# Kernel optimization log

Hardware: AMD Instinct MI355X
Metric: run time of the kernel (lower is better)

Reference implementation:

```python
import jax, jax.numpy as jnp
import numpy as np

DIM, H, KVH = 1024, 16, 4
HD = DIM // H            # head_dim = 64
KV_DIM = KVH * HD        # 256
ROPE_BASE = 10000.0
EPS = 1e-6


def setup_inputs() -> dict:
    key = jax.random.key(0)
    ks = jax.random.split(key, 6)
    B, S = 4, 2048
    x = jax.random.normal(ks[0], (B, S, DIM), dtype=jnp.float32)
    sc = 0.02
    Wq = jax.random.normal(ks[1], (DIM, DIM), dtype=jnp.float32) * sc
    Wk = jax.random.normal(ks[2], (KV_DIM, DIM), dtype=jnp.float32) * sc
    Wv = jax.random.normal(ks[3], (KV_DIM, DIM), dtype=jnp.float32) * sc
    Wo = jax.random.normal(ks[4], (DIM, DIM), dtype=jnp.float32) * sc
    q_gain = jnp.full((H,), 1.5, dtype=jnp.float32)
    return {"x": x, "Wq": Wq, "Wk": Wk, "Wv": Wv, "Wo": Wo, "q_gain": q_gain}


def _rms_norm(t):
    return t * jax.lax.rsqrt(jnp.mean(t * t, axis=-1, keepdims=True) + EPS)


def _rotary(seqlen, dtype):
    inv_freq = 1.0 / (ROPE_BASE ** (jnp.arange(0, HD, 2, dtype=jnp.float32) / HD))
    t = jnp.arange(seqlen, dtype=jnp.float32)
    freqs = jnp.outer(t, inv_freq)                      # [S, HD/2]
    return jnp.cos(freqs).astype(dtype)[None, None], jnp.sin(freqs).astype(dtype)[None, None]


def _apply_rot(t, cos, sin):
    half = t.shape[-1] // 2
    t1, t2 = t[..., :half], t[..., half:]
    return jnp.concatenate((t1 * cos + t2 * sin, -t1 * sin + t2 * cos), axis=-1)


def reference(x, Wq, Wk, Wv, Wo, q_gain):
    B, S, D = x.shape
    q = (x @ Wq.T).reshape(B, S, H, HD).transpose(0, 2, 1, 3)      # [B,H,S,HD]
    k = (x @ Wk.T).reshape(B, S, KVH, HD).transpose(0, 2, 1, 3)    # [B,KVH,S,HD]
    v = (x @ Wv.T).reshape(B, S, KVH, HD).transpose(0, 2, 1, 3)
    q, k = _rms_norm(q), _rms_norm(k)
    cos, sin = _rotary(S, q.dtype)
    q, k = _apply_rot(q, cos, sin), _apply_rot(k, cos, sin)
    q = q * q_gain.astype(q.dtype)[None, :, None, None]
    rep = H // KVH
    k_exp = jnp.repeat(k, rep, axis=1)                              # GQA expand
    v_exp = jnp.repeat(v, rep, axis=1)
    scores = jnp.einsum('bhqd,bhkd->bhqk', q, k_exp) / np.sqrt(HD)
    causal = jnp.tril(jnp.ones((S, S), dtype=bool))
    scores = jnp.where(causal[None, None], scores, jnp.finfo(scores.dtype).min)
    attn = jax.nn.softmax(scores, axis=-1)
    y = jnp.einsum('bhqk,bhkd->bhqd', attn, v_exp)
    y = y.transpose(0, 2, 1, 3).reshape(B, S, D)
    return y @ Wo.T
```

## Files before the change

### kernel.cpp

```cpp
#include <hip/hip_runtime.h>

typedef float f32x4 __attribute__((ext_vector_type(4)));
typedef float f32x16 __attribute__((ext_vector_type(16)));
typedef __bf16 bf16x8 __attribute__((ext_vector_type(8)));
typedef unsigned short u16x8 __attribute__((ext_vector_type(8)));
typedef int i32x2 __attribute__((ext_vector_type(2)));
typedef int i32x4 __attribute__((ext_vector_type(4)));

#define DEV static __device__ __forceinline__

DEV float bf2f(unsigned short h) {
  unsigned int u = ((unsigned int)h) << 16;
  return __builtin_bit_cast(float, u);
}
DEV unsigned short f2bf(float f) {
  unsigned int u = __builtin_bit_cast(unsigned int, f);
  u += 0x7fff + ((u >> 16) & 1);
  return (unsigned short)(u >> 16);
}

DEV void g2l16(const void* g, void* l) {
  __builtin_amdgcn_global_load_lds(
      (const __attribute__((address_space(1))) void*)g,
      (__attribute__((address_space(3))) void*)l, 16, 0, 0);
}

DEV unsigned int cvtpk(float lo, float hi) {
  unsigned int r;
  asm("v_cvt_pk_bf16_f32 %0, %1, %2" : "=v"(r) : "v"(lo), "v"(hi));
  return r;
}

DEV float fexp2(float x) {
  float r;
  asm("v_exp_f32 %0, %1" : "=v"(r) : "v"(x));
  return r;
}

DEV void cvt8(const float* __restrict__ in, unsigned short* __restrict__ out, int idx) {
  int i = idx * 8;
  float4 a = *(const float4*)(in + i);
  float4 b = *(const float4*)(in + i + 4);
  u16x8 r;
  r[0] = f2bf(a.x); r[1] = f2bf(a.y); r[2] = f2bf(a.z); r[3] = f2bf(a.w);
  r[4] = f2bf(b.x); r[5] = f2bf(b.y); r[6] = f2bf(b.z); r[7] = f2bf(b.w);
  *(u16x8*)(out + i) = r;
}

__global__ __launch_bounds__(256) void k_cvt_all(const float* __restrict__ x,
                                                 const float* __restrict__ wq,
                                                 const float* __restrict__ wk,
                                                 const float* __restrict__ wv,
                                                 const float* __restrict__ wo,
                                                 unsigned short* __restrict__ xb,
                                                 unsigned short* __restrict__ wcat,
                                                 unsigned short* __restrict__ wob,
                                                 float2* __restrict__ rope) {
  const int blk = blockIdx.x, tid = threadIdx.x;
  if (blk < 4096) {
    cvt8(x, xb, blk * 256 + tid);
  } else if (blk < 4608) {
    cvt8(wq, wcat, (blk - 4096) * 256 + tid);
  } else if (blk < 4736) {
    cvt8(wk, wcat + 1048576, (blk - 4608) * 256 + tid);
  } else if (blk < 4864) {
    cvt8(wv, wcat + 1310720, (blk - 4736) * 256 + tid);
  } else if (blk < 5376) {
    cvt8(wo, wob, (blk - 4864) * 256 + tid);
  } else {
    int idx = (blk - 5376) * 256 + tid;
    int s = idx >> 5, dmod = idx & 31;
    float inv_freq = powf(10000.0f, -(float)dmod * (1.0f / 32.0f));
    float sn, cs;
    sincosf((float)s * inv_freq, &sn, &cs);
    rope[idx] = make_float2(cs, sn);
  }
}

__global__ __launch_bounds__(256) void k_qkv(const unsigned short* __restrict__ A,
                                             const unsigned short* __restrict__ B,
                                             const float* __restrict__ qg,
                                             const float2* __restrict__ rope,
                                             unsigned short* __restrict__ qn,
                                             unsigned short* __restrict__ kn2,
                                             unsigned short* __restrict__ vt2) {
  __shared__ unsigned short LDS[16384];
  unsigned short* As = LDS;
  unsigned short* Bs = LDS + 8192;
  const int K = 1024;
  const int tid = threadIdx.x;
  const int wid = tid >> 6, lane = tid & 63;
  const int g = lane >> 4, r16 = lane & 15;
  const int m0 = blockIdx.x * 128;
  const int y = blockIdx.y;
  const int n0 = y * 128;
  const int wr = wid >> 1, wc = wid & 1;

  f32x4 acc[4][4];
#pragma unroll
  for (int i = 0; i < 4; ++i)
#pragma unroll
    for (int j = 0; j < 4; ++j) acc[i][j] = f32x4{0.f, 0.f, 0.f, 0.f};

  const int cb = (lane & 7) * 16;

  for (int k0 = 0; k0 < K; k0 += 64) {
#pragma unroll
    for (int c = 0; c < 4; ++c) {
      int i = wid * 4 + c;
      int row = i * 8 + (lane >> 3);
      int sc = cb ^ ((row & 7) << 4);
      g2l16((const char*)A + ((size_t)(m0 + row) * K + k0) * 2 + sc, (char*)As + i * 1024);
      g2l16((const char*)B + ((size_t)(n0 + row) * K + k0) * 2 + sc, (char*)Bs + i * 1024);
    }
    __syncthreads();
#pragma unroll
    for (int kh = 0; kh < 2; ++kh) {
      bf16x8 af[4], bfr[4];
#pragma unroll
      for (int m = 0; m < 4; ++m) {
        int row = wr * 64 + m * 16 + r16;
        int byte = row * 128 + ((g * 16 + kh * 64) ^ ((row & 7) << 4));
        af[m] = *(const bf16x8*)((const char*)As + byte);
      }
#pragma unroll
      for (int n = 0; n < 4; ++n) {
        int row = wc * 64 + n * 16 + r16;
        int byte = row * 128 + ((g * 16 + kh * 64) ^ ((row & 7) << 4));
        bfr[n] = *(const bf16x8*)((const char*)Bs + byte);
      }
#pragma unroll
      for (int m = 0; m < 4; ++m)
#pragma unroll
        for (int n = 0; n < 4; ++n)
          acc[m][n] = __builtin_amdgcn_mfma_f32_16x16x32_bf16(af[m], bfr[n], acc[m][n], 0, 0, 0);
    }
    __syncthreads();
  }

  if (y < 10) {
    const bool isq = (y < 8);
    const int head = isq ? (2 * y + wc) : (2 * (y - 8) + wc);
    const float gain = isq ? qg[head] * 0.18033688011112042f : 1.0f;
    unsigned short* T = LDS;
#pragma unroll
    for (int m = 0; m < 4; ++m)
#pragma unroll
      for (int j = 0; j < 4; ++j) {
        int tokl = wr * 64 + m * 16 + g * 4 + j;
        int tok = m0 + tokl;
        int s = tok & 2047;
        float v0 = acc[m][0][j], v1 = acc[m][1][j], v2 = acc[m][2][j], v3 = acc[m][3][j];
        float ss = v0 * v0 + v1 * v1 + v2 * v2 + v3 * v3;
        ss += __shfl_xor(ss, 1); ss += __shfl_xor(ss, 2);
        ss += __shfl_xor(ss, 4); ss += __shfl_xor(ss, 8);
        float rs = rsqrtf(ss * (1.0f / 64.0f) + 1e-6f) * gain;
        float2 cs0 = rope[s * 32 + r16];
        float2 cs1 = rope[s * 32 + 16 + r16];
        float o0 = (v0 * cs0.x + v2 * cs0.y) * rs;
        float o2 = (v2 * cs0.x - v0 * cs0.y) * rs;
        float o1 = (v1 * cs1.x + v3 * cs1.y) * rs;
        float o3 = (v3 * cs1.x - v1 * cs1.y) * rs;
        char* rowb = (char*)T + tokl * 256;
        const int sw = (tokl & 15) << 4;
        const int dbase = wc * 128 + r16 * 2;
        *(unsigned short*)(rowb + ((dbase) ^ sw)) = f2bf(o0);
        *(unsigned short*)(rowb + ((dbase + 32) ^ sw)) = f2bf(o1);
        *(unsigned short*)(rowb + ((dbase + 64) ^ sw)) = f2bf(o2);
        *(unsigned short*)(rowb + ((dbase + 96) ^ sw)) = f2bf(o3);
      }
    __syncthreads();
    if (isq) {
      const int row0 = tid >> 4, cl = tid & 15;
      unsigned short* dstb = qn + 2 * y * 64;
#pragma unroll
      for (int it = 0; it < 8; ++it) {
        int row = it * 16 + row0;
        i32x4 w = *(const i32x4*)((const char*)T + row * 256 + ((cl * 16) ^ ((row & 15) << 4)));
        *(i32x4*)(dstb + (size_t)(m0 + row) * 1024 + cl * 8) = w;
      }
    } else {
      const int b_ = m0 >> 11;
      const int kb0 = (m0 & 2047) >> 5;
      const int fu = tid >> 3, sub = tid & 7;
      const int hsel = fu >> 4, kb = (fu >> 2) & 3, m = fu & 3;
      const int headk = 2 * (y - 8) + hsel;
      unsigned short* dst =
          kn2 + ((size_t)((b_ * 4 + headk) * 64 + kb0 + kb) * 4 + m) * 512;
#pragma unroll
      for (int k = 0; k < 8; ++k) {
        int slot = k * 8 + sub;
        int kw = slot & 31, hi8 = slot >> 5;
        int tokl = kb * 32 + kw;
        int d0 = hsel * 64 + m * 16 + hi8 * 8;
        i32x4 w = *(const i32x4*)((const char*)T + tokl * 256 + ((d0 * 2) ^ ((tokl & 15) << 4)));
        *(i32x4*)(dst + slot * 8) = w;
      }
    }
  } else {
    unsigned short* T = LDS;
#pragma unroll
    for (int m = 0; m < 4; ++m)
#pragma unroll
      for (int n = 0; n < 4; ++n)
#pragma unroll
        for (int j = 0; j < 4; ++j) {
          int tokl = wr * 64 + m * 16 + g * 4 + j;
          int dl = wc * 64 + n * 16 + r16;
          int byte = (dl * 256 + tokl * 2) ^ ((dl & 15) << 4);
          *(unsigned short*)((char*)T + byte) = f2bf(acc[m][n][j]);
        }
    __syncthreads();
    const int d = tid >> 1, th = tid & 1;
    const int hv = 2 * (y - 10) + (d >> 6), dh = d & 63;
    const int bb = m0 >> 11;
    const int s0 = (m0 & 2047) + th * 64;
    const int kb64 = s0 >> 6;
    const int db = dh >> 5, d31 = dh & 31;
    const size_t vb0 = ((size_t)(bb * 4 + hv) * 32 + kb64) * 8 + db * 4;
    const int swz = (d & 15) << 4;
#pragma unroll
    for (int c = 0; c < 8; ++c) {
      i32x4 w = *(const i32x4*)((const char*)T + ((d * 256 + th * 128 + c * 16) ^ swz));
      *(i32x4*)(vt2 + (vb0 + (c >> 1)) * 512 + ((c & 1) * 32 + d31) * 8) = w;
    }
  }
}

__global__ __launch_bounds__(256) void k_gemm_bt(const unsigned short* __restrict__ A,
                                                 const unsigned short* __restrict__ B,
                                                 float* __restrict__ C, int M, int N, int K) {
  __shared__ unsigned short As[128 * 64];
  __shared__ unsigned short Bs[128 * 64];
  const int tid = threadIdx.x;
  const int wid = tid >> 6, lane = tid & 63;
  const int g = lane >> 4, r16 = lane & 15;
  const int m0 = blockIdx.x * 128, n0 = blockIdx.y * 128;
  const int wr = wid >> 1, wc = wid & 1;

  f32x4 acc[4][4];
#pragma unroll
  for (int i = 0; i < 4; ++i)
#pragma unroll
    for (int j = 0; j < 4; ++j) acc[i][j] = f32x4{0.f, 0.f, 0.f, 0.f};

  const int cb = (lane & 7) * 16;

  for (int k0 = 0; k0 < K; k0 += 64) {
#pragma unroll
    for (int c = 0; c < 4; ++c) {
      int i = wid * 4 + c;
      int row = i * 8 + (lane >> 3);
      int sc = cb ^ ((row & 7) << 4);
      g2l16((const char*)A + ((size_t)(m0 + row) * K + k0) * 2 + sc, (char*)As + i * 1024);
      g2l16((const char*)B + ((size_t)(n0 + row) * K + k0) * 2 + sc, (char*)Bs + i * 1024);
    }
    __syncthreads();
#pragma unroll
    for (int kh = 0; kh < 2; ++kh) {
      bf16x8 af[4], bfr[4];
#pragma unroll
      for (int m = 0; m < 4; ++m) {
        int row = wr * 64 + m * 16 + r16;
        int byte = row * 128 + ((g * 16 + kh * 64) ^ ((row & 7) << 4));
        af[m] = *(const bf16x8*)((const char*)As + byte);
      }
#pragma unroll
      for (int n = 0; n < 4; ++n) {
        int row = wc * 64 + n * 16 + r16;
        int byte = row * 128 + ((g * 16 + kh * 64) ^ ((row & 7) << 4));
        bfr[n] = *(const bf16x8*)((const char*)Bs + byte);
      }
#pragma unroll
      for (int m = 0; m < 4; ++m)
#pragma unroll
        for (int n = 0; n < 4; ++n)
          acc[m][n] = __builtin_amdgcn_mfma_f32_16x16x32_bf16(af[m], bfr[n], acc[m][n], 0, 0, 0);
    }
    __syncthreads();
  }
#pragma unroll
  for (int m = 0; m < 4; ++m)
#pragma unroll
    for (int n = 0; n < 4; ++n)
#pragma unroll
      for (int j = 0; j < 4; ++j) {
        int row = m0 + wr * 64 + m * 16 + g * 4 + j;
        int col = n0 + wc * 64 + n * 16 + r16;
        C[(size_t)row * N + col] = acc[m][n][j];
      }
}

__global__ __launch_bounds__(512) void k_attn2(const unsigned short* __restrict__ qn,
                                               const unsigned short* __restrict__ kn2,
                                               const unsigned short* __restrict__ vt2,
                                               unsigned short* __restrict__ yb) {
  __shared__ unsigned short SMEM[4 * 8192];
  const int tid = threadIdx.x;
  const int wid = tid >> 6, lane = tid & 63;
  const int hi = lane >> 5, l31 = lane & 31;
  const int flat = blockIdx.x;
  const int qcx = 7 - (flat >> 6);
  const int bh = flat & 63;
  const int b = bh >> 4, h = bh & 15, hv = h >> 2;
  const int q0w = qcx * 256 + wid * 32;
  const int qglob = q0w + l31;
  const int tdiag = (q0w + 31) >> 6;
  const size_t tok0 = (size_t)b * 2048;

  const u16x8 onesu = {0x3F80, 0x3F80, 0x3F80, 0x3F80, 0x3F80, 0x3F80, 0x3F80, 0x3F80};
  const bf16x8 ones = __builtin_bit_cast(bf16x8, onesu);

  bf16x8 qf[4];
#pragma unroll
  for (int m = 0; m < 4; ++m)
    qf[m] = *(const bf16x8*)(qn + (tok0 + qglob) * 1024 + h * 64 + m * 16 + hi * 8);

  f32x16 oacc[2], lacc, zer;
#pragma unroll
  for (int r = 0; r < 16; ++r) { oacc[0][r] = 0.f; oacc[1][r] = 0.f; lacc[r] = 0.f; zer[r] = 0.f; }

  const int c0 = wid * 2;
  const unsigned short* src0;
  if (wid < 4) {
    src0 = kn2 + (size_t)(b * 4 + hv) * 131072 + c0 * 512 + lane * 8;
  } else {
    src0 = vt2 + (size_t)(b * 4 + hv) * 131072 + (c0 - 8) * 512 + lane * 8;
  }
  const unsigned short* src1 = src0 + 512;

  auto stage = [&](int T, int tb) {
    char* dst = (char*)SMEM + tb * 16384 + c0 * 1024;
    g2l16(src0 + (size_t)T * 4096, dst);
    g2l16(src1 + (size_t)T * 4096, dst + 1024);
  };

  const char* lbase = (const char*)SMEM + lane * 16;

  auto qk_tile = [&](int tb, f32x16* s) {
    const char* base = lbase + tb * 16384;
#pragma unroll
    for (int kt = 0; kt < 2; ++kt) {
      __builtin_amdgcn_s_setprio(1);
      bf16x8 kf = *(const bf16x8*)(base + (kt * 4) * 1024);
      f32x16 a = __builtin_amdgcn_mfma_f32_32x32x16_bf16(kf, qf[0], zer, 0, 0, 0);
#pragma unroll
      for (int m = 1; m < 4; ++m) {
        kf = *(const bf16x8*)(base + (kt * 4 + m) * 1024);
        a = __builtin_amdgcn_mfma_f32_32x32x16_bf16(kf, qf[m], a, 0, 0, 0);
      }
      __builtin_amdgcn_s_setprio(0);
      s[kt] = a;
    }
  };

  auto mask_tile = [&](int t, f32x16* s) {
    const int k0 = t * 64;
#pragma unroll
    for (int kt = 0; kt < 2; ++kt)
#pragma unroll
      for (int r = 0; r < 16; ++r) {
        int key = k0 + kt * 32 + (r & 3) + 8 * (r >> 2) + 4 * hi;
        if (key > qglob) s[kt][r] = -INFINITY;
      }
  };

  auto softmax_cvt = [&](f32x16* s, i32x4* paw) {
#pragma unroll
    for (int kt = 0; kt < 2; ++kt)
#pragma unroll
      for (int r = 0; r < 16; ++r) s[kt][r] = fexp2(s[kt][r]);
#pragma unroll
    for (int kt = 0; kt < 2; ++kt)
#pragma unroll
      for (int half = 0; half < 2; ++half) {
        int bs = half * 8;
        unsigned int a0 = cvtpk(s[kt][bs + 0], s[kt][bs + 1]);
        unsigned int a1 = cvtpk(s[kt][bs + 2], s[kt][bs + 3]);
        unsigned int b0 = cvtpk(s[kt][bs + 4], s[kt][bs + 5]);
        unsigned int b1 = cvtpk(s[kt][bs + 6], s[kt][bs + 7]);
        i32x2 r0 = __builtin_amdgcn_permlane32_swap((int)a0, (int)b0, false, false);
        i32x2 r1 = __builtin_amdgcn_permlane32_swap((int)a1, (int)b1, false, false);
        i32x4 w;
        w[0] = r0[0]; w[1] = r1[0]; w[2] = r0[1]; w[3] = r1[1];
        paw[kt * 2 + half] = w;
      }
  };

  auto pv_tile = [&](int tb, const i32x4* paw) {
    const char* base = lbase + tb * 16384 + 8192;
    __builtin_amdgcn_s_setprio(1);
#pragma unroll
    for (int db = 0; db < 2; ++db)
#pragma unroll
      for (int ks = 0; ks < 4; ++ks) {
        bf16x8 vf = *(const bf16x8*)(base + (db * 4 + ks) * 1024);
        oacc[db] = __builtin_amdgcn_mfma_f32_32x32x16_bf16(
            vf, __builtin_bit_cast(bf16x8, paw[ks]), oacc[db], 0, 0, 0);
      }
#pragma unroll
    for (int ks = 0; ks < 4; ++ks)
      lacc = __builtin_amdgcn_mfma_f32_32x32x16_bf16(
          ones, __builtin_bit_cast(bf16x8, paw[ks]), lacc, 0, 0, 0);
    __builtin_amdgcn_s_setprio(0);
  };

  const int npair = 2 * qcx + 2;

  stage(0, 0);
  stage(1, 1);
  __syncthreads();

  for (int p = 0; p < npair; ++p) {
    const int pb = (p & 1) << 1;
    if (p + 1 < npair) {
      stage(2 * p + 2, pb ^ 2);
      stage(2 * p + 3, (pb ^ 2) | 1);
    }
    const int t0 = 2 * p;
    const bool visa = (t0 <= tdiag), visb = (t0 + 1 <= tdiag);
    const bool domask = (p >= npair - 2);
    f32x16 sa[2], sb[2];
    if (visa) qk_tile(pb, sa);
    if (visb) qk_tile(pb | 1, sb);
    if (domask) {
      if (visa) mask_tile(t0, sa);
      if (visb) mask_tile(t0 + 1, sb);
    }
    i32x4 pawa[4], pawb[4];
    if (visa) {
      softmax_cvt(sa, pawa);
      pv_tile(pb, pawa);
    }
    if (visb) {
      softmax_cvt(sb, pawb);
      pv_tile(pb | 1, pawb);
    }
    __syncthreads();
  }

  const float inv = 1.0f / lacc[0];
  const int swl = (l31 & 7) << 4;
  char* obase = (char*)SMEM + wid * 4096;
#pragma unroll
  for (int db = 0; db < 2; ++db)
#pragma unroll
    for (int i = 0; i < 8; ++i) {
      int r = 2 * i;
      int dim = db * 32 + (r & 3) + 8 * (r >> 2) + 4 * hi;
      unsigned int w = (unsigned int)f2bf(oacc[db][r] * inv) |
                       ((unsigned int)f2bf(oacc[db][r + 1] * inv) << 16);
      *(unsigned int*)(obase + l31 * 128 + ((dim * 2) ^ swl)) = w;
    }
  __syncthreads();
#pragma unroll
  for (int it = 0; it < 4; ++it) {
    int cc = it * 2 + hi;
    i32x4 w = *(const i32x4*)(obase + l31 * 128 + ((cc * 16) ^ swl));
    *(i32x4*)(yb + (tok0 + q0w + l31) * 1024 + h * 64 + cc * 8) = w;
  }
}

extern "C" void kernel_launch(void* const* d_in, const int* in_sizes, int n_in,
                              void* d_out, int out_size, void* d_ws, size_t ws_size,
                              hipStream_t stream) {
  (void)in_sizes; (void)n_in; (void)out_size; (void)ws_size;
  const float* x  = (const float*)d_in[0];
  const float* Wq = (const float*)d_in[1];
  const float* Wk = (const float*)d_in[2];
  const float* Wv = (const float*)d_in[3];
  const float* Wo = (const float*)d_in[4];
  const float* qg = (const float*)d_in[5];

  char* ws = (char*)d_ws;
  unsigned short* xb   = (unsigned short*)(ws);
  unsigned short* wcat = (unsigned short*)(ws + 16777216);
  unsigned short* wob  = (unsigned short*)(ws + 19922944);
  unsigned short* qn   = (unsigned short*)(ws + 22020096);
  unsigned short* kn2  = (unsigned short*)(ws + 38797312);
  unsigned short* yb   = xb;
  unsigned short* vt2  = (unsigned short*)((char*)d_out + 25165824);
  float2*         rope = (float2*)((char*)d_out + 29360128);

  k_cvt_all<<<5632, 256, 0, stream>>>(x, Wq, Wk, Wv, Wo, xb, wcat, wob, rope);
  k_qkv<<<dim3(64, 12), 256, 0, stream>>>(xb, wcat, qg, rope, qn, kn2, vt2);
  k_attn2<<<512, 512, 0, stream>>>(qn, kn2, vt2, yb);
  k_gemm_bt<<<dim3(64, 8), 256, 0, stream>>>(yb, wob, (float*)d_out, 8192, 1024, 1024);
}
```

Measured before the change: 132.7 us.

## Shrink attention blocks to 128 queries with single-tile double buffering

Measured after the change: 140.7 us. 6.0% more time.

```diff
diff --git a/kernel.cpp b/kernel.cpp
--- a/kernel.cpp
+++ b/kernel.cpp
@@ -291,19 +291,19 @@
       }
 }
 
-__global__ __launch_bounds__(512) void k_attn2(const unsigned short* __restrict__ qn,
+__global__ __launch_bounds__(256) void k_attn2(const unsigned short* __restrict__ qn,
                                                const unsigned short* __restrict__ kn2,
                                                const unsigned short* __restrict__ vt2,
                                                unsigned short* __restrict__ yb) {
-  __shared__ unsigned short SMEM[4 * 8192];
+  __shared__ unsigned short SMEM[2 * 8192];
   const int tid = threadIdx.x;
   const int wid = tid >> 6, lane = tid & 63;
   const int hi = lane >> 5, l31 = lane & 31;
   const int flat = blockIdx.x;
-  const int qcx = 7 - (flat >> 6);
+  const int qx = 15 - (flat >> 6);
   const int bh = flat & 63;
   const int b = bh >> 4, h = bh & 15, hv = h >> 2;
-  const int q0w = qcx * 256 + wid * 32;
+  const int q0w = qx * 128 + wid * 32;
   const int qglob = q0w + l31;
   const int tdiag = (q0w + 31) >> 6;
   const size_t tok0 = (size_t)b * 2048;
@@ -320,19 +320,15 @@
 #pragma unroll
   for (int r = 0; r < 16; ++r) { oacc[0][r] = 0.f; oacc[1][r] = 0.f; lacc[r] = 0.f; zer[r] = 0.f; }
 
-  const int c0 = wid * 2;
-  const unsigned short* src0;
-  if (wid < 4) {
-    src0 = kn2 + (size_t)(b * 4 + hv) * 131072 + c0 * 512 + lane * 8;
-  } else {
-    src0 = vt2 + (size_t)(b * 4 + hv) * 131072 + (c0 - 8) * 512 + lane * 8;
-  }
-  const unsigned short* src1 = src0 + 512;
+  const unsigned short* srcb =
+      ((wid < 2) ? kn2 : vt2) + (size_t)(b * 4 + hv) * 131072 + ((wid & 1) * 4) * 512 + lane * 8;
+  const int dstoff = ((wid & 2) << 12) + (wid & 1) * 4096;
 
   auto stage = [&](int T, int tb) {
-    char* dst = (char*)SMEM + tb * 16384 + c0 * 1024;
-    g2l16(src0 + (size_t)T * 4096, dst);
-    g2l16(src1 + (size_t)T * 4096, dst + 1024);
+    char* dst = (char*)SMEM + tb * 16384 + dstoff;
+    const unsigned short* s = srcb + (size_t)T * 4096;
+#pragma unroll
+    for (int f = 0; f < 4; ++f) g2l16(s + f * 512, dst + f * 1024);
   };
 
   const char* lbase = (const char*)SMEM + lane * 16;
@@ -405,36 +401,21 @@
     __builtin_amdgcn_s_setprio(0);
   };
 
-  const int npair = 2 * qcx + 2;
+  const int nt = 2 * qx + 2;
 
   stage(0, 0);
-  stage(1, 1);
   __syncthreads();
 
-  for (int p = 0; p < npair; ++p) {
-    const int pb = (p & 1) << 1;
-    if (p + 1 < npair) {
-      stage(2 * p + 2, pb ^ 2);
-      stage(2 * p + 3, (pb ^ 2) | 1);
-    }
-    const int t0 = 2 * p;
-    const bool visa = (t0 <= tdiag), visb = (t0 + 1 <= tdiag);
-    const bool domask = (p >= npair - 2);
-    f32x16 sa[2], sb[2];
-    if (visa) qk_tile(pb, sa);
-    if (visb) qk_tile(pb | 1, sb);
-    if (domask) {
-      if (visa) mask_tile(t0, sa);
-      if (visb) mask_tile(t0 + 1, sb);
-    }
-    i32x4 pawa[4], pawb[4];
-    if (visa) {
-      softmax_cvt(sa, pawa);
-      pv_tile(pb, pawa);
-    }
-    if (visb) {
-      softmax_cvt(sb, pawb);
-      pv_tile(pb | 1, pawb);
+  for (int t = 0; t < nt; ++t) {
+    const int cur = t & 1;
+    if (t + 1 < nt) stage(t + 1, cur ^ 1);
+    if (t <= tdiag) {
+      f32x16 s[2];
+      qk_tile(cur, s);
+      if (t >= nt - 2) mask_tile(t, s);
+      i32x4 paw[4];
+      softmax_cvt(s, paw);
+      pv_tile(cur, paw);
     }
     __syncthreads();
   }
@@ -484,6 +465,6 @@
 
   k_cvt_all<<<5632, 256, 0, stream>>>(x, Wq, Wk, Wv, Wo, xb, wcat, wob, rope);
   k_qkv<<<dim3(64, 12), 256, 0, stream>>>(xb, wcat, qg, rope, qn, kn2, vt2);
-  k_attn2<<<512, 512, 0, stream>>>(qn, kn2, vt2, yb);
+  k_attn2<<<1024, 256, 0, stream>>>(qn, kn2, vt2, yb);
   k_gemm_bt<<<dim3(64, 8), 256, 0, stream>>>(yb, wob, (float*)d_out, 8192, 1024, 1024);
 }
```
